# Kernel tuning notes

Hardware: AMD Instinct MI355X
Metric: run time of the kernel (lower is better)

Reference implementation:

```python
import jax, jax.numpy as jnp
import numpy as np

DIM = 1024
NUM_HEADS = 16
HEAD_DIM = DIM // NUM_HEADS
SCALE = HEAD_DIM ** -0.5
B, N = 2, 2048


def setup_inputs() -> dict:
    key = jax.random.key(0)
    k_x, k_qkv, k_prjw, k_prjb = jax.random.split(key, 4)
    # nn.Linear(dim, 3*dim, bias=False): weight [3*dim, dim]
    s = 1.0 / np.sqrt(DIM)
    return {
        "x": jax.random.normal(k_x, (B, N, DIM), dtype=jnp.float32),
        "w_qkv": jax.random.uniform(k_qkv, (3 * DIM, DIM), jnp.float32, -s, s),
        "w_prj": jax.random.uniform(k_prjw, (DIM, DIM), jnp.float32, -s, s),
        "b_prj": jax.random.uniform(k_prjb, (DIM,), jnp.float32, -s, s),
    }


def reference(x, w_qkv, w_prj, b_prj):
    Bb, Nn, C = x.shape
    qkv = jnp.einsum("bnc,dc->bnd", x, w_qkv)            # [B,N,3C]
    qkv = qkv.reshape(Bb, Nn, 3, NUM_HEADS, HEAD_DIM)
    qkv = jnp.transpose(qkv, (2, 0, 3, 1, 4))            # [3,B,H,N,hd]
    q, k, v = qkv[0], qkv[1], qkv[2]
    attn = jnp.einsum("bhqd,bhkd->bhqk", q, k) * SCALE   # [B,H,N,N]
    attn = jax.nn.softmax(attn, axis=-1)
    out = jnp.einsum("bhqk,bhkd->bhqd", attn, v)         # [B,H,N,hd]
    out = jnp.transpose(out, (0, 2, 1, 3)).reshape(Bb, Nn, C)
    # dropout layers are identity at eval / p=0
    return jnp.einsum("bnc,dc->bnd", out, w_prj) + b_prj
```

## Files before the change

kernel.cpp:

```cpp
#include <hip/hip_runtime.h>

typedef unsigned short u16;
typedef unsigned int u32;
typedef __attribute__((ext_vector_type(8))) short s16x8;
typedef __attribute__((ext_vector_type(4))) short s16x4;
typedef __attribute__((ext_vector_type(4))) float f32x4;

#define DIM    1024
#define NHEADS 16
#define HD     64
#define NSEQ   2048
#define QKVN   3072

__device__ __forceinline__ u16 f2bf(float f) {
  u32 u = __float_as_uint(f);
  u += 0x7FFF + ((u >> 16) & 1);
  return (u16)(u >> 16);
}

__device__ __forceinline__ float vexp2(float x) {
#if __has_builtin(__builtin_amdgcn_exp2f)
  return __builtin_amdgcn_exp2f(x);
#else
  return __expf(x * 0.69314718055994531f);
#endif
}

__device__ __forceinline__ void async16(const u16* g, u16* l) {
  __builtin_amdgcn_global_load_lds(
      (const __attribute__((address_space(1))) unsigned int*)g,
      (__attribute__((address_space(3))) unsigned int*)l, 16, 0, 0);
}

__global__ void cast_all(const float* __restrict__ x, const float* __restrict__ wq,
                         const float* __restrict__ wp, u16* __restrict__ xo,
                         u16* __restrict__ wqo, u16* __restrict__ wpo) {
  int i = blockIdx.x * 256 + threadIdx.x;
  const float4* src; u16* dst; int off;
  if (i < 1048576)      { src = (const float4*)x;  dst = xo;  off = i; }
  else if (i < 1835008) { src = (const float4*)wq; dst = wqo; off = i - 1048576; }
  else                  { src = (const float4*)wp; dst = wpo; off = i - 1835008; }
  float4 f = src[off];
  ushort4 o;
  o.x = f2bf(f.x); o.y = f2bf(f.y); o.z = f2bf(f.z); o.w = f2bf(f.w);
  ((ushort4*)dst)[off] = o;
}

template <bool FINAL>
__global__ __launch_bounds__(256, 3) void gemm_bt(
    const u16* __restrict__ A, const u16* __restrict__ Bw, u16* __restrict__ qkv,
    u16* __restrict__ vt, const float* __restrict__ bias, float* __restrict__ outp) {
  constexpr int K = 1024;
  constexpr int BM = FINAL ? 64 : 128;
  constexpr int MT = FINAL ? 64 : 32;
  constexpr int IT = FINAL ? 2 : 4;
  constexpr int ACALLS = BM / 16;
  constexpr int TCALLS = ACALLS + 8;
  constexpr int PW = TCALLS / 4;
  const int bm = blockIdx.x % MT;
  const int bn = blockIdx.x / MT;
  const int tid = threadIdx.x;
  const int wave = tid >> 6, lane = tid & 63;
  const int q4 = lane >> 4, l15 = lane & 15;
  const int wm = wave >> 1, wn = wave & 1;
  const int m0 = bm * BM, n0 = bn * 128;

  __shared__ alignas(16) u16 lsA[2][BM * 32];
  __shared__ alignas(16) u16 lsB[2][128 * 32];

  f32x4 acc[IT][4];
#pragma unroll
  for (int i = 0; i < IT; i++)
#pragma unroll
    for (int j = 0; j < 4; j++) acc[i][j] = (f32x4){0.f, 0.f, 0.f, 0.f};

  auto stage = [&](int k0, int buf) {
#pragma unroll
    for (int j = 0; j < PW; ++j) {
      int t = wave * PW + j;
      if (t < ACALLS) {
        int lin = t * 64 + lane;
        int r = lin >> 2, c = lin & 3;
        async16(A + (size_t)(m0 + r) * K + k0 + c * 8, lsA[buf] + t * 512);
      } else {
        int tb = t - ACALLS;
        int lin = tb * 64 + lane;
        int r = lin >> 2, c = lin & 3;
        async16(Bw + (size_t)(n0 + r) * K + k0 + c * 8, lsB[buf] + tb * 512);
      }
    }
  };

  stage(0, 0);

  for (int k0 = 0; k0 < K; k0 += 32) {
    const int buf = (k0 >> 5) & 1;
    __syncthreads();
    if (k0 + 32 < K) stage(k0 + 32, buf ^ 1);
    s16x8 af[IT], bfr[4];
#pragma unroll
    for (int i = 0; i < IT; ++i)
      af[i] = *(const s16x8*)(lsA[buf] + (wm * (IT * 16) + i * 16 + l15) * 32 + q4 * 8);
#pragma unroll
    for (int j = 0; j < 4; ++j)
      bfr[j] = *(const s16x8*)(lsB[buf] + (wn * 64 + j * 16 + l15) * 32 + q4 * 8);
    __builtin_amdgcn_s_setprio(1);
#pragma unroll
    for (int i = 0; i < IT; ++i)
#pragma unroll
      for (int j = 0; j < 4; ++j)
        acc[i][j] = __builtin_amdgcn_mfma_f32_16x16x32_bf16(af[i], bfr[j], acc[i][j], 0, 0, 0);
    __builtin_amdgcn_s_setprio(0);
  }

#pragma unroll
  for (int i = 0; i < IT; i++) {
#pragma unroll
    for (int j = 0; j < 4; j++) {
      int n = n0 + wn * 64 + j * 16 + l15;
      int mb = m0 + wm * (IT * 16) + i * 16 + q4 * 4;
      if (FINAL) {
#pragma unroll
        for (int r = 0; r < 4; r++)
          outp[(size_t)(mb + r) * DIM + n] = acc[i][j][r] + bias[n];
      } else if (n < 2048) {
#pragma unroll
        for (int r = 0; r < 4; r++)
          qkv[(size_t)(mb + r) * QKVN + n] = f2bf(acc[i][j][r]);
      } else {
        int b = mb >> 11, tok = mb & 2047;
        int h = (n >> 6) & 15, hd = n & 63;
        ushort4 pk;
        pk.x = f2bf(acc[i][j][0]); pk.y = f2bf(acc[i][j][1]);
        pk.z = f2bf(acc[i][j][2]); pk.w = f2bf(acc[i][j][3]);
        *(ushort4*)(vt + ((size_t)((b * NHEADS + h) * HD + hd)) * NSEQ + tok) = pk;
      }
    }
  }
}

__global__ __launch_bounds__(256, 2) void attn_kernel(const u16* __restrict__ qkv,
                                                      const u16* __restrict__ vt,
                                                      u16* __restrict__ aout) {
  const int blk = blockIdx.x;
  const int bh = blk & 31, qt = blk >> 5;
  const int b = bh >> 4, h = bh & 15;
  const int tid = threadIdx.x;
  const int wave = tid >> 6, lane = tid & 63;
  const int g = wave >> 1, wq = wave & 1;
  const int q4 = lane >> 4, l15 = lane & 15;

  __shared__ alignas(16) u16 smem[32768];
  u16* lsKb = smem + g * 2 * 4096;
  u16* lsVb = smem + 16384 + g * 2 * 4096;
  float* lsO = (float*)smem;
  float* lsS = lsO + 64 * 132;

  const float QSCALE = 0.18033688011112042f;
  s16x8 aq[4][2];
#pragma unroll
  for (int rt = 0; rt < 4; ++rt)
#pragma unroll
    for (int kc = 0; kc < 2; ++kc) {
      int row = b * NSEQ + qt * 128 + wq * 64 + rt * 16 + l15;
      uint4 d = *(const uint4*)(qkv + (size_t)row * QKVN + h * HD + kc * 32 + q4 * 8);
      u32 w[4] = {d.x, d.y, d.z, d.w};
      s16x8 f;
#pragma unroll
      for (int j = 0; j < 8; ++j) {
        u16 u = (u16)(w[j >> 1] >> ((j & 1) * 16));
        float v = __uint_as_float(((u32)u) << 16) * QSCALE;
        f[j] = (short)f2bf(v);
      }
      aq[rt][kc] = f;
    }

  f32x4 o[4][4];
  float lsum[4] = {0.f, 0.f, 0.f, 0.f};
#pragma unroll
  for (int rt = 0; rt < 4; ++rt)
#pragma unroll
    for (int ht = 0; ht < 4; ++ht) o[rt][ht] = (f32x4){0.f, 0.f, 0.f, 0.f};

  auto stage = [&](int ktl, int buf) {
#pragma unroll
    for (int j = 0; j < 4; ++j) {
      int t = wq * 4 + j;
      int lin = t * 64 + lane;
      int r = lin >> 3, c = (lin & 7) ^ (r & 7);
      int key = g * 1024 + ktl * 64;
      async16(qkv + (size_t)(b * NSEQ + key + r) * QKVN + DIM + h * HD + c * 8,
              lsKb + buf * 4096 + t * 512);
      async16(vt + (size_t)(bh * HD + r) * NSEQ + key + c * 8,
              lsVb + buf * 4096 + t * 512);
    }
  };

  stage(0, 0);

  for (int kt = 0; kt < 16; ++kt) {
    const int buf = kt & 1;
    __syncthreads();
    if (kt + 1 < 16) stage(kt + 1, buf ^ 1);
    const u16* lsK = lsKb + buf * 4096;
    const u16* lsV = lsVb + buf * 4096;

    s16x8 kf[2][4];
#pragma unroll
    for (int kc = 0; kc < 2; ++kc)
#pragma unroll
      for (int ct = 0; ct < 4; ++ct) {
        int r = ct * 16 + l15;
        int c = (kc * 4 + q4) ^ (r & 7);
        kf[kc][ct] = *(const s16x8*)(lsK + r * 64 + c * 8);
      }
    s16x8 vf8[2][4];
#pragma unroll
    for (int c = 0; c < 2; ++c)
#pragma unroll
      for (int ht = 0; ht < 4; ++ht) {
        int row = ht * 16 + l15;
        int ch0 = c * 4 + (q4 >> 1);
        int ch1 = ch0 + 2;
        union { s16x4 hh[2]; s16x8 v; } u;
        u.hh[0] = *(const s16x4*)(lsV + row * 64 + (ch0 ^ (row & 7)) * 8 + (q4 & 1) * 4);
        u.hh[1] = *(const s16x4*)(lsV + row * 64 + (ch1 ^ (row & 7)) * 8 + (q4 & 1) * 4);
        vf8[c][ht] = u.v;
      }

#pragma unroll
    for (int rt = 0; rt < 4; ++rt) {
      f32x4 st[4];
#pragma unroll
      for (int ct = 0; ct < 4; ++ct) st[ct] = (f32x4){0.f, 0.f, 0.f, 0.f};
#pragma unroll
      for (int kc = 0; kc < 2; ++kc)
#pragma unroll
        for (int ct = 0; ct < 4; ++ct)
          st[ct] = __builtin_amdgcn_mfma_f32_16x16x32_bf16(kf[kc][ct], aq[rt][kc], st[ct], 0, 0, 0);

      s16x8 pa8[2];
#pragma unroll
      for (int c = 0; c < 2; ++c) {
        union { u32 w[4]; s16x8 v; } pk;
#pragma unroll
        for (int h2 = 0; h2 < 2; ++h2) {
          int ct = c * 2 + h2;
          u32 u0 = __float_as_uint(vexp2(st[ct][0]));
          u32 u1 = __float_as_uint(vexp2(st[ct][1]));
          u32 u2 = __float_as_uint(vexp2(st[ct][2]));
          u32 u3 = __float_as_uint(vexp2(st[ct][3]));
          lsum[rt] += __uint_as_float(u0 & 0xffff0000u) + __uint_as_float(u1 & 0xffff0000u) +
                      __uint_as_float(u2 & 0xffff0000u) + __uint_as_float(u3 & 0xffff0000u);
          pk.w[h2 * 2 + 0] = (u0 >> 16) | (u1 & 0xffff0000u);
          pk.w[h2 * 2 + 1] = (u2 >> 16) | (u3 & 0xffff0000u);
        }
        pa8[c] = pk.v;
      }

#pragma unroll
      for (int c = 0; c < 2; ++c)
#pragma unroll
        for (int ht = 0; ht < 4; ++ht)
          o[rt][ht] = __builtin_amdgcn_mfma_f32_16x16x32_bf16(pa8[c], vf8[c][ht], o[rt][ht], 0, 0, 0);
    }
  }

#pragma unroll
  for (int rt = 0; rt < 4; ++rt) {
    lsum[rt] += __shfl_xor(lsum[rt], 16, 64);
    lsum[rt] += __shfl_xor(lsum[rt], 32, 64);
  }

  __syncthreads();
  if (g == 1) {
#pragma unroll
    for (int rt = 0; rt < 4; ++rt) {
#pragma unroll
      for (int ht = 0; ht < 4; ++ht) {
        int addr = (ht * 16 + l15) * 132 + wq * 64 + rt * 16 + q4 * 4;
        *(float4*)(lsO + addr) = (float4){o[rt][ht][0], o[rt][ht][1], o[rt][ht][2], o[rt][ht][3]};
      }
      if (q4 == 0) lsS[wq * 64 + rt * 16 + l15] = lsum[rt];
    }
  }
  __syncthreads();
  if (g == 0) {
#pragma unroll
    for (int rt = 0; rt < 4; ++rt) {
      float4 s2 = *(const float4*)(lsS + wq * 64 + rt * 16 + q4 * 4);
      float inv[4];
      inv[0] = 1.0f / (__shfl(lsum[rt], q4 * 4 + 0, 64) + s2.x);
      inv[1] = 1.0f / (__shfl(lsum[rt], q4 * 4 + 1, 64) + s2.y);
      inv[2] = 1.0f / (__shfl(lsum[rt], q4 * 4 + 2, 64) + s2.z);
      inv[3] = 1.0f / (__shfl(lsum[rt], q4 * 4 + 3, 64) + s2.w);
#pragma unroll
      for (int ht = 0; ht < 4; ++ht) {
        float4 o2 = *(const float4*)(lsO + (ht * 16 + l15) * 132 + wq * 64 + rt * 16 + q4 * 4);
        float v[4] = {o[rt][ht][0] + o2.x, o[rt][ht][1] + o2.y,
                      o[rt][ht][2] + o2.z, o[rt][ht][3] + o2.w};
#pragma unroll
        for (int r = 0; r < 4; ++r) {
          int n = qt * 128 + wq * 64 + rt * 16 + q4 * 4 + r;
          int col = h * HD + ht * 16 + l15;
          aout[(size_t)(b * NSEQ + n) * DIM + col] = f2bf(v[r] * inv[r]);
        }
      }
    }
  }
}

extern "C" void kernel_launch(void* const* d_in, const int* in_sizes, int n_in,
                              void* d_out, int out_size, void* d_ws, size_t ws_size,
                              hipStream_t stream) {
  const float* x     = (const float*)d_in[0];
  const float* w_qkv = (const float*)d_in[1];
  const float* w_prj = (const float*)d_in[2];
  const float* b_prj = (const float*)d_in[3];
  float* out = (float*)d_out;

  char* ws = (char*)d_ws;
  u16* x_bf    = (u16*)(ws);
  u16* wqkv_bf = (u16*)(ws + (size_t)(8u << 20));
  u16* wprj_bf = (u16*)(ws + (size_t)(14u << 20));
  u16* qkv     = (u16*)(ws + (size_t)(16u << 20));
  u16* vt      = (u16*)(ws + (size_t)(40u << 20));
  u16* aout    = (u16*)(ws + (size_t)(48u << 20));

  cast_all<<<8192, 256, 0, stream>>>(x, w_qkv, w_prj, x_bf, wqkv_bf, wprj_bf);
  gemm_bt<false><<<32 * 24, 256, 0, stream>>>(x_bf, wqkv_bf, qkv, vt, nullptr, nullptr);
  attn_kernel<<<512, 256, 0, stream>>>(qkv, vt, aout);
  gemm_bt<true><<<64 * 8, 256, 0, stream>>>(aout, wprj_bf, nullptr, nullptr, b_prj, out);
}
```

Before: 176.0 us.

## Double attention block to 512 threads with 32 query rows per wave

The attention kernel now launches 8 waves per block instead of 4, so each wave handles 32 query rows instead of 64, which halves its per-wave accumulator and Q-fragment registers. The inner loop is split into two halves over the key tile so fewer K/V fragments are live at once. Staging is redistributed so half the waves load K and half load V. The aim is more waves in flight per CU to hide latency, at the cost of reading K/V fragments from LDS twice as often per query row and more barrier participants.

```diff
diff --git a/kernel.cpp b/kernel.cpp
--- a/kernel.cpp
+++ b/kernel.cpp
@@ -139,7 +139,7 @@
   }
 }
 
-__global__ __launch_bounds__(256, 2) void attn_kernel(const u16* __restrict__ qkv,
+__global__ __launch_bounds__(512, 2) void attn_kernel(const u16* __restrict__ qkv,
                                                       const u16* __restrict__ vt,
                                                       u16* __restrict__ aout) {
   const int blk = blockIdx.x;
@@ -147,7 +147,7 @@
   const int b = bh >> 4, h = bh & 15;
   const int tid = threadIdx.x;
   const int wave = tid >> 6, lane = tid & 63;
-  const int g = wave >> 1, wq = wave & 1;
+  const int g = wave >> 2, wq = wave & 3;
   const int q4 = lane >> 4, l15 = lane & 15;
 
   __shared__ alignas(16) u16 smem[32768];
@@ -157,12 +157,12 @@
   float* lsS = lsO + 64 * 132;
 
   const float QSCALE = 0.18033688011112042f;
-  s16x8 aq[4][2];
-#pragma unroll
-  for (int rt = 0; rt < 4; ++rt)
+  s16x8 aq[2][2];
+#pragma unroll
+  for (int rt = 0; rt < 2; ++rt)
 #pragma unroll
     for (int kc = 0; kc < 2; ++kc) {
-      int row = b * NSEQ + qt * 128 + wq * 64 + rt * 16 + l15;
+      int row = b * NSEQ + qt * 128 + wq * 32 + rt * 16 + l15;
       uint4 d = *(const uint4*)(qkv + (size_t)row * QKVN + h * HD + kc * 32 + q4 * 8);
       u32 w[4] = {d.x, d.y, d.z, d.w};
       s16x8 f;
@@ -175,24 +175,27 @@
       aq[rt][kc] = f;
     }
 
-  f32x4 o[4][4];
-  float lsum[4] = {0.f, 0.f, 0.f, 0.f};
-#pragma unroll
-  for (int rt = 0; rt < 4; ++rt)
+  f32x4 o[2][4];
+  float lsum[2] = {0.f, 0.f};
+#pragma unroll
+  for (int rt = 0; rt < 2; ++rt)
 #pragma unroll
     for (int ht = 0; ht < 4; ++ht) o[rt][ht] = (f32x4){0.f, 0.f, 0.f, 0.f};
 
   auto stage = [&](int ktl, int buf) {
 #pragma unroll
     for (int j = 0; j < 4; ++j) {
-      int t = wq * 4 + j;
+      int id = wq * 4 + j;
+      int t = id & 7;
       int lin = t * 64 + lane;
       int r = lin >> 3, c = (lin & 7) ^ (r & 7);
       int key = g * 1024 + ktl * 64;
-      async16(qkv + (size_t)(b * NSEQ + key + r) * QKVN + DIM + h * HD + c * 8,
-              lsKb + buf * 4096 + t * 512);
-      async16(vt + (size_t)(bh * HD + r) * NSEQ + key + c * 8,
-              lsVb + buf * 4096 + t * 512);
+      if (id < 8)
+        async16(qkv + (size_t)(b * NSEQ + key + r) * QKVN + DIM + h * HD + c * 8,
+                lsKb + buf * 4096 + t * 512);
+      else
+        async16(vt + (size_t)(bh * HD + r) * NSEQ + key + c * 8,
+                lsVb + buf * 4096 + t * 512);
     }
   };
 
@@ -205,69 +208,66 @@
     const u16* lsK = lsKb + buf * 4096;
     const u16* lsV = lsVb + buf * 4096;
 
-    s16x8 kf[2][4];
-#pragma unroll
-    for (int kc = 0; kc < 2; ++kc)
-#pragma unroll
-      for (int ct = 0; ct < 4; ++ct) {
-        int r = ct * 16 + l15;
-        int c = (kc * 4 + q4) ^ (r & 7);
-        kf[kc][ct] = *(const s16x8*)(lsK + r * 64 + c * 8);
-      }
-    s16x8 vf8[2][4];
-#pragma unroll
-    for (int c = 0; c < 2; ++c)
+#pragma unroll
+    for (int hf = 0; hf < 2; ++hf) {
+      s16x8 kf[2][2];
+#pragma unroll
+      for (int kc = 0; kc < 2; ++kc)
+#pragma unroll
+        for (int ctl = 0; ctl < 2; ++ctl) {
+          int r = (hf * 2 + ctl) * 16 + l15;
+          int c = (kc * 4 + q4) ^ (r & 7);
+          kf[kc][ctl] = *(const s16x8*)(lsK + r * 64 + c * 8);
+        }
+      s16x8 vf8[4];
 #pragma unroll
       for (int ht = 0; ht < 4; ++ht) {
         int row = ht * 16 + l15;
-        int ch0 = c * 4 + (q4 >> 1);
+        int ch0 = hf * 4 + (q4 >> 1);
         int ch1 = ch0 + 2;
         union { s16x4 hh[2]; s16x8 v; } u;
         u.hh[0] = *(const s16x4*)(lsV + row * 64 + (ch0 ^ (row & 7)) * 8 + (q4 & 1) * 4);
         u.hh[1] = *(const s16x4*)(lsV + row * 64 + (ch1 ^ (row & 7)) * 8 + (q4 & 1) * 4);
-        vf8[c][ht] = u.v;
-      }
-
-#pragma unroll
-    for (int rt = 0; rt < 4; ++rt) {
-      f32x4 st[4];
-#pragma unroll
-      for (int ct = 0; ct < 4; ++ct) st[ct] = (f32x4){0.f, 0.f, 0.f, 0.f};
-#pragma unroll
-      for (int kc = 0; kc < 2; ++kc)
-#pragma unroll
-        for (int ct = 0; ct < 4; ++ct)
-          st[ct] = __builtin_amdgcn_mfma_f32_16x16x32_bf16(kf[kc][ct], aq[rt][kc], st[ct], 0, 0, 0);
-
-      s16x8 pa8[2];
-#pragma unroll
-      for (int c = 0; c < 2; ++c) {
-        union { u32 w[4]; s16x8 v; } pk;
-#pragma unroll
-        for (int h2 = 0; h2 < 2; ++h2) {
-          int ct = c * 2 + h2;
-          u32 u0 = __float_as_uint(vexp2(st[ct][0]));
-          u32 u1 = __float_as_uint(vexp2(st[ct][1]));
-          u32 u2 = __float_as_uint(vexp2(st[ct][2]));
-          u32 u3 = __float_as_uint(vexp2(st[ct][3]));
-          lsum[rt] += __uint_as_float(u0 & 0xffff0000u) + __uint_as_float(u1 & 0xffff0000u) +
-                      __uint_as_float(u2 & 0xffff0000u) + __uint_as_float(u3 & 0xffff0000u);
-          pk.w[h2 * 2 + 0] = (u0 >> 16) | (u1 & 0xffff0000u);
-          pk.w[h2 * 2 + 1] = (u2 >> 16) | (u3 & 0xffff0000u);
+        vf8[ht] = u.v;
+      }
+
+#pragma unroll
+      for (int rt = 0; rt < 2; ++rt) {
+        f32x4 st[2];
+#pragma unroll
+        for (int ctl = 0; ctl < 2; ++ctl) st[ctl] = (f32x4){0.f, 0.f, 0.f, 0.f};
+#pragma unroll
+        for (int kc = 0; kc < 2; ++kc)
+#pragma unroll
+          for (int ctl = 0; ctl < 2; ++ctl)
+            st[ctl] = __builtin_amdgcn_mfma_f32_16x16x32_bf16(kf[kc][ctl], aq[rt][kc], st[ctl], 0, 0, 0);
+
+        s16x8 pa8;
+        {
+          union { u32 w[4]; s16x8 v; } pk;
+#pragma unroll
+          for (int h2 = 0; h2 < 2; ++h2) {
+            u32 u0 = __float_as_uint(vexp2(st[h2][0]));
+            u32 u1 = __float_as_uint(vexp2(st[h2][1]));
+            u32 u2 = __float_as_uint(vexp2(st[h2][2]));
+            u32 u3 = __float_as_uint(vexp2(st[h2][3]));
+            lsum[rt] += __uint_as_float(u0 & 0xffff0000u) + __uint_as_float(u1 & 0xffff0000u) +
+                        __uint_as_float(u2 & 0xffff0000u) + __uint_as_float(u3 & 0xffff0000u);
+            pk.w[h2 * 2 + 0] = (u0 >> 16) | (u1 & 0xffff0000u);
+            pk.w[h2 * 2 + 1] = (u2 >> 16) | (u3 & 0xffff0000u);
+          }
+          pa8 = pk.v;
         }
-        pa8[c] = pk.v;
-      }
-
-#pragma unroll
-      for (int c = 0; c < 2; ++c)
+
 #pragma unroll
         for (int ht = 0; ht < 4; ++ht)
-          o[rt][ht] = __builtin_amdgcn_mfma_f32_16x16x32_bf16(pa8[c], vf8[c][ht], o[rt][ht], 0, 0, 0);
-    }
-  }
-
-#pragma unroll
-  for (int rt = 0; rt < 4; ++rt) {
+          o[rt][ht] = __builtin_amdgcn_mfma_f32_16x16x32_bf16(pa8, vf8[ht], o[rt][ht], 0, 0, 0);
+      }
+    }
+  }
+
+#pragma unroll
+  for (int rt = 0; rt < 2; ++rt) {
     lsum[rt] += __shfl_xor(lsum[rt], 16, 64);
     lsum[rt] += __shfl_xor(lsum[rt], 32, 64);
   }
@@ -275,20 +275,20 @@
   __syncthreads();
   if (g == 1) {
 #pragma unroll
-    for (int rt = 0; rt < 4; ++rt) {
+    for (int rt = 0; rt < 2; ++rt) {
 #pragma unroll
       for (int ht = 0; ht < 4; ++ht) {
-        int addr = (ht * 16 + l15) * 132 + wq * 64 + rt * 16 + q4 * 4;
+        int addr = (ht * 16 + l15) * 132 + wq * 32 + rt * 16 + q4 * 4;
         *(float4*)(lsO + addr) = (float4){o[rt][ht][0], o[rt][ht][1], o[rt][ht][2], o[rt][ht][3]};
       }
-      if (q4 == 0) lsS[wq * 64 + rt * 16 + l15] = lsum[rt];
+      if (q4 == 0) lsS[wq * 32 + rt * 16 + l15] = lsum[rt];
     }
   }
   __syncthreads();
   if (g == 0) {
 #pragma unroll
-    for (int rt = 0; rt < 4; ++rt) {
-      float4 s2 = *(const float4*)(lsS + wq * 64 + rt * 16 + q4 * 4);
+    for (int rt = 0; rt < 2; ++rt) {
+      float4 s2 = *(const float4*)(lsS + wq * 32 + rt * 16 + q4 * 4);
       float inv[4];
       inv[0] = 1.0f / (__shfl(lsum[rt], q4 * 4 + 0, 64) + s2.x);
       inv[1] = 1.0f / (__shfl(lsum[rt], q4 * 4 + 1, 64) + s2.y);
@@ -296,12 +296,12 @@
       inv[3] = 1.0f / (__shfl(lsum[rt], q4 * 4 + 3, 64) + s2.w);
 #pragma unroll
       for (int ht = 0; ht < 4; ++ht) {
-        float4 o2 = *(const float4*)(lsO + (ht * 16 + l15) * 132 + wq * 64 + rt * 16 + q4 * 4);
+        float4 o2 = *(const float4*)(lsO + (ht * 16 + l15) * 132 + wq * 32 + rt * 16 + q4 * 4);
         float v[4] = {o[rt][ht][0] + o2.x, o[rt][ht][1] + o2.y,
                       o[rt][ht][2] + o2.z, o[rt][ht][3] + o2.w};
 #pragma unroll
         for (int r = 0; r < 4; ++r) {
-          int n = qt * 128 + wq * 64 + rt * 16 + q4 * 4 + r;
+          int n = qt * 128 + wq * 32 + rt * 16 + q4 * 4 + r;
           int col = h * HD + ht * 16 + l15;
           aout[(size_t)(b * NSEQ + n) * DIM + col] = f2bf(v[r] * inv[r]);
         }
@@ -329,6 +329,6 @@
 
   cast_all<<<8192, 256, 0, stream>>>(x, w_qkv, w_prj, x_bf, wqkv_bf, wprj_bf);
   gemm_bt<false><<<32 * 24, 256, 0, stream>>>(x_bf, wqkv_bf, qkv, vt, nullptr, nullptr);
-  attn_kernel<<<512, 256, 0, stream>>>(qkv, vt, aout);
+  attn_kernel<<<512, 512, 0, stream>>>(qkv, vt, aout);
   gemm_bt<true><<<64 * 8, 256, 0, stream>>>(aout, wprj_bf, nullptr, nullptr, b_prj, out);
 }
```

New measurement: 178.3 us. About the same (+1.3%).
